# Kernel optimization log

Hardware: AMD Instinct MI355X
Metric: run time of the kernel (lower is better)

## Reference

```python
import jax, jax.numpy as jnp
import numpy as np

SIZES = [(1362944, 123904), (123904, 11264), (11264, 1024)]  # (n_src, n_tgt) per hop
FANOUT = 10
IN_CH, HID, OUT_CH = 128, 256, 47
BN_EPS = 1e-5


def setup_inputs() -> dict:
    key = jax.random.key(0)
    ks = iter(jax.random.split(key, 64))
    inp = {"x": jax.random.normal(next(ks), (SIZES[0][0], IN_CH), jnp.float32)}
    for i, (ns, nt) in enumerate(SIZES):
        e = nt * FANOUT
        src = jax.random.randint(next(ks), (e,), 0, ns, dtype=jnp.int32)
        tgt = jax.random.randint(next(ks), (e,), 0, nt, dtype=jnp.int32)
        inp[f"ei{i}"] = jnp.stack([src, tgt])  # [2, E]
    dins = [IN_CH, HID, HID]
    for i, din in enumerate(dins):
        inp[f"c{i}_w1"] = jax.random.normal(next(ks), (din, HID), jnp.float32) * (2.0 / din) ** 0.5
        inp[f"c{i}_b1"] = jnp.zeros((HID,), jnp.float32)
        inp[f"c{i}_g"] = jnp.ones((HID,), jnp.float32)
        inp[f"c{i}_be"] = jnp.zeros((HID,), jnp.float32)
        inp[f"c{i}_w2"] = jax.random.normal(next(ks), (HID, HID), jnp.float32) * (2.0 / HID) ** 0.5
        inp[f"c{i}_b2"] = jnp.zeros((HID,), jnp.float32)
    inp["lin1_w"] = jax.random.normal(next(ks), (HID, HID), jnp.float32) * (1.0 / HID) ** 0.5
    inp["lin1_b"] = jnp.zeros((HID,), jnp.float32)
    inp["lin2_w"] = jax.random.normal(next(ks), (HID, OUT_CH), jnp.float32) * (1.0 / HID) ** 0.5
    inp["lin2_b"] = jnp.zeros((OUT_CH,), jnp.float32)
    return inp


def _gin_layer(x, ei, n_tgt, w1, b1, g, be, w2, b2):
    # GINConv(eps=0): h = MLP(x_target + sum_{j->i} x_j)
    x_tgt = x[:n_tgt]
    msg = jax.ops.segment_sum(x[ei[0]], ei[1], num_segments=n_tgt)
    h = x_tgt + msg
    h = h @ w1 + b1
    mu = jnp.mean(h, axis=0)
    var = jnp.var(h, axis=0)  # biased, as in torch BN training mode
    h = (h - mu) * jax.lax.rsqrt(var + BN_EPS) * g + be
    h = jax.nn.relu(h)
    h = jax.nn.relu(h @ w2 + b2)
    return h


def reference(x, ei0, ei1, ei2,
              c0_w1, c0_b1, c0_g, c0_be, c0_w2, c0_b2,
              c1_w1, c1_b1, c1_g, c1_be, c1_w2, c1_b2,
              c2_w1, c2_b1, c2_g, c2_be, c2_w2, c2_b2,
              lin1_w, lin1_b, lin2_w, lin2_b):
    eis = [ei0, ei1, ei2]
    params = [(c0_w1, c0_b1, c0_g, c0_be, c0_w2, c0_b2),
              (c1_w1, c1_b1, c1_g, c1_be, c1_w2, c1_b2),
              (c2_w1, c2_b1, c2_g, c2_be, c2_w2, c2_b2)]
    h = x
    for i, (_, n_tgt) in enumerate(SIZES):
        h = _gin_layer(h, eis[i], n_tgt, *params[i])
    h = jax.nn.relu(h @ lin1_w + lin1_b)
    # dropout(p=0.5) is identity in eval mode
    h = h @ lin2_w + lin2_b
    return jax.nn.log_softmax(h, axis=-1)
```

## Files before the change

### kernel.cpp

```cpp
#include <hip/hip_runtime.h>
#include <cmath>

typedef _Float16 f16;
typedef _Float16 half8 __attribute__((ext_vector_type(8)));
typedef _Float16 half4 __attribute__((ext_vector_type(4)));
typedef float f32x4 __attribute__((ext_vector_type(4)));

__device__ __forceinline__ void atomAddF(float* p, float v) { unsafeAtomicAdd(p, v); }

__device__ __forceinline__ void gload16(const void* g, void* l) {
    __builtin_amdgcn_global_load_lds((const __attribute__((address_space(1))) void*)g,
                                     (__attribute__((address_space(3))) void*)l, 16, 0, 0);
}

struct SetupP {
    const float* ws[7];
    f16* wd[7];
    const float* l2s;
    float* l2d;
    float* stats;
    int* deg;
};

__global__ void setup_all(SetupP p) {
    int i = blockIdx.x * 256 + threadIdx.x;
    if (i < 32768) {
        int k = i >> 8, n = i & 255;
        p.wd[0][(size_t)n * 128 + k] = (f16)p.ws[0][i];
        return;
    }
    i -= 32768;
    if (i < 6 * 65536) {
        int m = i >> 16, r = i & 65535;
        int k = r >> 8, n = r & 255;
        p.wd[1 + m][(size_t)n * 256 + k] = (f16)p.ws[1 + m][r];
        return;
    }
    i -= 6 * 65536;
    if (i < 12032) {
        int k = i / 47, j = i - k * 47;
        p.l2d[(size_t)j * 256 + k] = p.l2s[i];
        return;
    }
    i -= 12032;
    if (i < 1536) {
        p.stats[i] = 0.f;
        return;
    }
    i -= 1536;
    if (i < 136192) p.deg[i] = 0;
}

__global__ void fill_all(const int* __restrict__ e0, const int* __restrict__ e1,
                         const int* __restrict__ e2, int E0, int E1, int E2, int* __restrict__ deg,
                         int* __restrict__ adj) {
    int e = blockIdx.x * 256 + threadIdx.x;
    const int *src, *tgt;
    int* d;
    int* a;
    if (e < E0) {
        src = e0; tgt = e0 + E0; d = deg; a = adj;
    } else if (e < E0 + E1) {
        e -= E0;
        src = e1; tgt = e1 + E1; d = deg + 123904; a = adj + (size_t)123904 * 64;
    } else if (e < E0 + E1 + E2) {
        e -= E0 + E1;
        src = e2; tgt = e2 + E2; d = deg + 135168; a = adj + (size_t)135168 * 64;
    } else {
        return;
    }
    int t = tgt[e];
    int pos = atomicAdd(&d[t], 1);
    if (pos < 64) a[(size_t)t * 64 + pos] = src[e];
}


__global__ void gather128(const float* __restrict__ x, const int* __restrict__ deg,
                          const int* __restrict__ adj, f16* __restrict__ h) {
    const int wave = threadIdx.x >> 6, lane = threadIdx.x & 63;
    const int row = blockIdx.x * 4 + wave;
    const int c = lane * 2;
    const float* xr = x + (size_t)row * 128 + c;
    float a0 = xr[0], a1 = xr[1];
    const int n = min(deg[row], 64);
    const int myadj = adj[(size_t)row * 64 + lane];
    int j = 0;
    for (; j + 4 <= n; j += 4) {
        int s0 = __shfl(myadj, j), s1 = __shfl(myadj, j + 1);
        int s2 = __shfl(myadj, j + 2), s3 = __shfl(myadj, j + 3);
        const float* p0 = x + (size_t)s0 * 128 + c;
        const float* p1 = x + (size_t)s1 * 128 + c;
        const float* p2 = x + (size_t)s2 * 128 + c;
        const float* p3 = x + (size_t)s3 * 128 + c;
        float b00 = p0[0], b01 = p0[1], b10 = p1[0], b11 = p1[1];
        float b20 = p2[0], b21 = p2[1], b30 = p3[0], b31 = p3[1];
        a0 += (b00 + b10) + (b20 + b30);
        a1 += (b01 + b11) + (b21 + b31);
    }
    for (; j < n; ++j) {
        int s = __shfl(myadj, j);
        const float* p = x + (size_t)s * 128 + c;
        a0 += p[0];
        a1 += p[1];
    }
    f16* hp = h + (size_t)row * 128 + c;
    hp[0] = (f16)a0;
    hp[1] = (f16)a1;
}

__global__ void gather256(const f16* __restrict__ x, const int* __restrict__ deg,
                          const int* __restrict__ adj, f16* __restrict__ h) {
    const int wave = threadIdx.x >> 6, lane = threadIdx.x & 63;
    const int row = blockIdx.x * 4 + wave;
    const int c = lane * 4;
    half4 xv = *(const half4*)(x + (size_t)row * 256 + c);
    float a0 = (float)xv[0], a1 = (float)xv[1], a2 = (float)xv[2], a3 = (float)xv[3];
    const int n = min(deg[row], 64);
    const int myadj = adj[(size_t)row * 64 + lane];
    int j = 0;
    for (; j + 4 <= n; j += 4) {
        int s0 = __shfl(myadj, j), s1 = __shfl(myadj, j + 1);
        int s2 = __shfl(myadj, j + 2), s3 = __shfl(myadj, j + 3);
        half4 v0 = *(const half4*)(x + (size_t)s0 * 256 + c);
        half4 v1 = *(const half4*)(x + (size_t)s1 * 256 + c);
        half4 v2 = *(const half4*)(x + (size_t)s2 * 256 + c);
        half4 v3 = *(const half4*)(x + (size_t)s3 * 256 + c);
        a0 += ((float)v0[0] + (float)v1[0]) + ((float)v2[0] + (float)v3[0]);
        a1 += ((float)v0[1] + (float)v1[1]) + ((float)v2[1] + (float)v3[1]);
        a2 += ((float)v0[2] + (float)v1[2]) + ((float)v2[2] + (float)v3[2]);
        a3 += ((float)v0[3] + (float)v1[3]) + ((float)v2[3] + (float)v3[3]);
    }
    for (; j < n; ++j) {
        int s = __shfl(myadj, j);
        half4 v = *(const half4*)(x + (size_t)s * 256 + c);
        a0 += (float)v[0];
        a1 += (float)v[1];
        a2 += (float)v[2];
        a3 += (float)v[3];
    }
    half4 o;
    o[0] = (f16)a0;
    o[1] = (f16)a1;
    o[2] = (f16)a2;
    o[3] = (f16)a3;
    *(half4*)(h + (size_t)row * 256 + c) = o;
}

__global__ __launch_bounds__(256) void gemm128_stats(const f16* __restrict__ A,
                                                     const f16* __restrict__ Bt,
                                                     const float* __restrict__ bias,
                                                     f16* __restrict__ C,
                                                     float* __restrict__ colsum,
                                                     float* __restrict__ colsumsq, int M, int N,
                                                     int K) {
    __shared__ __attribute__((aligned(16))) f16 sA[128 * 32];
    __shared__ __attribute__((aligned(16))) f16 sB[128 * 32];
    __shared__ float ssum[128], ssq[128];
    const int tid = threadIdx.x;
    const int wave = tid >> 6, lane = tid & 63;
    const int quad = lane >> 4, l16 = lane & 15;
    const int wr = (wave & 1) * 64, wc = (wave >> 1) * 64;
    const int row0 = blockIdx.x * 128, col0 = blockIdx.y * 128;

    if (tid < 128)
        ssum[tid] = 0.f;
    else
        ssq[tid - 128] = 0.f;

    const int i0 = tid, i1 = tid + 256;
    const int r0s = i0 >> 2, c0s = (i0 & 3) ^ ((r0s >> 1) & 3);
    const int r1s = i1 >> 2, c1s = (i1 & 3) ^ ((r1s >> 1) & 3);
    const f16* ga0 = A + (size_t)(row0 + r0s) * K + c0s * 8;
    const f16* ga1 = A + (size_t)(row0 + r1s) * K + c1s * 8;
    const f16* gb0 = Bt + (size_t)(col0 + r0s) * K + c0s * 8;
    const f16* gb1 = Bt + (size_t)(col0 + r1s) * K + c1s * 8;
    f16* la0 = &sA[i0 * 8];
    f16* la1 = &sA[i1 * 8];
    f16* lb0 = &sB[i0 * 8];
    f16* lb1 = &sB[i1 * 8];

    f32x4 acc[4][4] = {};

    for (int k0 = 0; k0 < K; k0 += 32) {
        __syncthreads();
        gload16(ga0 + k0, la0);
        gload16(ga1 + k0, la1);
        gload16(gb0 + k0, lb0);
        gload16(gb1 + k0, lb1);
        __syncthreads();
        half8 af[4], bf[4];
#pragma unroll
        for (int r = 0; r < 4; ++r) {
            const int ar = wr + r * 16 + l16;
            af[r] = *(const half8*)&sA[ar * 32 + ((quad ^ ((ar >> 1) & 3)) * 8)];
        }
#pragma unroll
        for (int c = 0; c < 4; ++c) {
            const int br = wc + c * 16 + l16;
            bf[c] = *(const half8*)&sB[br * 32 + ((quad ^ ((br >> 1) & 3)) * 8)];
        }
#pragma unroll
        for (int r = 0; r < 4; ++r)
#pragma unroll
            for (int c = 0; c < 4; ++c)
                acc[r][c] = __builtin_amdgcn_mfma_f32_16x16x32_f16(af[r], bf[c], acc[r][c], 0, 0, 0);
    }

#pragma unroll
    for (int c = 0; c < 4; ++c) {
        const int lcol = wc + c * 16 + l16;
        const int gcol = col0 + lcol;
        const float b = bias[gcol];
        float cs = 0.f, cq = 0.f;
#pragma unroll
        for (int r = 0; r < 4; ++r) {
#pragma unroll
            for (int i = 0; i < 4; ++i) {
                const int grow = row0 + wr + r * 16 + quad * 4 + i;
                float v = acc[r][c][i] + b;
                C[(size_t)grow * N + gcol] = (f16)v;
                cs += v;
                cq += v * v;
            }
        }
        cs += __shfl_xor(cs, 16);
        cs += __shfl_xor(cs, 32);
        cq += __shfl_xor(cq, 16);
        cq += __shfl_xor(cq, 32);
        if (quad == 0) {
            atomicAdd(&ssum[lcol], cs);
            atomicAdd(&ssq[lcol], cq);
        }
    }
    __syncthreads();
    if (tid < 128)
        atomAddF(&colsum[col0 + tid], ssum[tid]);
    else
        atomAddF(&colsumsq[col0 + tid - 128], ssq[tid - 128]);
}

__global__ __launch_bounds__(256) void gemm128_bn(const f16* __restrict__ A,
                                                  const f16* __restrict__ Bt,
                                                  const float* __restrict__ bias,
                                                  const float* __restrict__ colsum,
                                                  const float* __restrict__ colsumsq,
                                                  const float* __restrict__ g,
                                                  const float* __restrict__ be, float nt_inv,
                                                  f16* __restrict__ C, int M, int N, int K) {
    __shared__ __attribute__((aligned(16))) f16 sA[128 * 32];
    __shared__ __attribute__((aligned(16))) f16 sB[128 * 32];
    __shared__ float s_scale[256], s_shift[256];
    const int tid = threadIdx.x;
    const int wave = tid >> 6, lane = tid & 63;
    const int quad = lane >> 4, l16 = lane & 15;
    const int wr = (wave & 1) * 64, wc = (wave >> 1) * 64;
    const int row0 = blockIdx.x * 128, col0 = blockIdx.y * 128;

    {
        float mu = colsum[tid] * nt_inv;
        float var = colsumsq[tid] * nt_inv - mu * mu;
        float sc = g[tid] * rsqrtf(var + 1e-5f);
        s_scale[tid] = sc;
        s_shift[tid] = be[tid] - mu * sc;
    }
    __syncthreads();

    const int i0 = tid, i1 = tid + 256;
    const int r0s = i0 >> 2, c0s = (i0 & 3) ^ ((r0s >> 1) & 3);
    const int r1s = i1 >> 2, c1s = (i1 & 3) ^ ((r1s >> 1) & 3);
    const f16* ga0 = A + (size_t)(row0 + r0s) * K + c0s * 8;
    const f16* ga1 = A + (size_t)(row0 + r1s) * K + c1s * 8;
    const f16* gb0 = Bt + (size_t)(col0 + r0s) * K + c0s * 8;
    const f16* gb1 = Bt + (size_t)(col0 + r1s) * K + c1s * 8;
    f16* la0 = &sA[i0 * 8];
    f16* la1 = &sA[i1 * 8];
    f16* lb0 = &sB[i0 * 8];
    f16* lb1 = &sB[i1 * 8];

    f32x4 acc[4][4] = {};

    for (int k0 = 0; k0 < K; k0 += 32) {
        half8 va0 = *(const half8*)(ga0 + k0);
        half8 va1 = *(const half8*)(ga1 + k0);
        half8 ta0, ta1;
        const int kb0 = k0 + c0s * 8, kb1 = k0 + c1s * 8;
#pragma unroll
        for (int j = 0; j < 8; ++j) {
            float f0 = (float)va0[j] * s_scale[kb0 + j] + s_shift[kb0 + j];
            ta0[j] = (f16)fmaxf(f0, 0.f);
            float f1 = (float)va1[j] * s_scale[kb1 + j] + s_shift[kb1 + j];
            ta1[j] = (f16)fmaxf(f1, 0.f);
        }
        __syncthreads();
        gload16(gb0 + k0, lb0);
        gload16(gb1 + k0, lb1);
        *(half8*)la0 = ta0;
        *(half8*)la1 = ta1;
        __syncthreads();
        half8 af[4], bf[4];
#pragma unroll
        for (int r = 0; r < 4; ++r) {
            const int ar = wr + r * 16 + l16;
            af[r] = *(const half8*)&sA[ar * 32 + ((quad ^ ((ar >> 1) & 3)) * 8)];
        }
#pragma unroll
        for (int c = 0; c < 4; ++c) {
            const int br = wc + c * 16 + l16;
            bf[c] = *(const half8*)&sB[br * 32 + ((quad ^ ((br >> 1) & 3)) * 8)];
        }
#pragma unroll
        for (int r = 0; r < 4; ++r)
#pragma unroll
            for (int c = 0; c < 4; ++c)
                acc[r][c] = __builtin_amdgcn_mfma_f32_16x16x32_f16(af[r], bf[c], acc[r][c], 0, 0, 0);
    }

#pragma unroll
    for (int c = 0; c < 4; ++c) {
        const int gcol = col0 + wc + c * 16 + l16;
        const float b = bias[gcol];
#pragma unroll
        for (int r = 0; r < 4; ++r) {
#pragma unroll
            for (int i = 0; i < 4; ++i) {
                const int grow = row0 + wr + r * 16 + quad * 4 + i;
                float v = fmaxf(acc[r][c][i] + b, 0.f);
                C[(size_t)grow * N + gcol] = (f16)v;
            }
        }
    }
}

template <bool RELU>
__global__ __launch_bounds__(256) void gemm_bt(const f16* __restrict__ A, const f16* __restrict__ Bt,
                                               const float* __restrict__ bias, f16* __restrict__ C,
                                               int M, int N, int K) {
    constexpr int BM = 64, BN = 64, BK = 32, LP = 40;
    __shared__ f16 sA[BM * LP];
    __shared__ f16 sB[BN * LP];
    const int tid = threadIdx.x;
    const int wave = tid >> 6, lane = tid & 63;
    const int quad = lane >> 4, l16 = lane & 15;
    const int wr = (wave & 1) * 32, wc = (wave >> 1) * 32;
    const int row0 = blockIdx.x * BM, col0 = blockIdx.y * BN;
    const int srow = tid >> 2, soff = (tid & 3) * 8;

    f32x4 acc[2][2] = {};

    for (int k0 = 0; k0 < K; k0 += BK) {
        __syncthreads();
        *(half8*)&sA[srow * LP + soff] =
            *(const half8*)(A + (size_t)(row0 + srow) * K + (k0 + soff));
        *(half8*)&sB[srow * LP + soff] =
            *(const half8*)(Bt + (size_t)(col0 + srow) * K + (k0 + soff));
        __syncthreads();
        half8 af[2], bf[2];
#pragma unroll
        for (int r = 0; r < 2; ++r) af[r] = *(const half8*)&sA[(wr + r * 16 + l16) * LP + quad * 8];
#pragma unroll
        for (int c = 0; c < 2; ++c) bf[c] = *(const half8*)&sB[(wc + c * 16 + l16) * LP + quad * 8];
#pragma unroll
        for (int r = 0; r < 2; ++r)
#pragma unroll
            for (int c = 0; c < 2; ++c)
                acc[r][c] = __builtin_amdgcn_mfma_f32_16x16x32_f16(af[r], bf[c], acc[r][c], 0, 0, 0);
    }

#pragma unroll
    for (int c = 0; c < 2; ++c) {
        const int gcol = col0 + wc + c * 16 + l16;
        const float b = bias[gcol];
#pragma unroll
        for (int r = 0; r < 2; ++r) {
#pragma unroll
            for (int i = 0; i < 4; ++i) {
                const int grow = row0 + wr + r * 16 + quad * 4 + i;
                float v = acc[r][c][i] + b;
                if (RELU) v = fmaxf(v, 0.f);
                C[(size_t)grow * N + gcol] = (f16)v;
            }
        }
    }
}

__global__ void head2(const f16* __restrict__ T, const float* __restrict__ w2t,
                      const float* __restrict__ b2, float* __restrict__ out, int rows) {
    const int row = blockIdx.x;
    const int lane = threadIdx.x;
    __shared__ float tr[256];
    for (int i = lane; i < 256; i += 64) tr[i] = (float)T[(size_t)row * 256 + i];
    __syncthreads();
    float d = -1e30f;
    if (lane < 47) {
        const float* wr = w2t + (size_t)lane * 256;
        float dot = 0.f;
        for (int k = 0; k < 256; k += 4) {
            dot += tr[k] * wr[k] + tr[k + 1] * wr[k + 1] + tr[k + 2] * wr[k + 2] +
                   tr[k + 3] * wr[k + 3];
        }
        d = dot + b2[lane];
    }
    float m = d;
    for (int off = 32; off; off >>= 1) m = fmaxf(m, __shfl_xor(m, off));
    float e = (lane < 47) ? expf(d - m) : 0.f;
    float s = e;
    for (int off = 32; off; off >>= 1) s += __shfl_xor(s, off);
    if (lane < 47) out[(size_t)row * 47 + lane] = d - m - logf(s);
}


extern "C" void kernel_launch(void* const* d_in, const int* in_sizes, int n_in, void* d_out,
                              int out_size, void* d_ws, size_t ws_size, hipStream_t stream) {
    const float* x0 = (const float*)d_in[0];
    const int* ei[3] = {(const int*)d_in[1], (const int*)d_in[2], (const int*)d_in[3]};
    const int E[3] = {in_sizes[1] / 2, in_sizes[2] / 2, in_sizes[3] / 2};
    const float* c_w1[3] = {(const float*)d_in[4], (const float*)d_in[10], (const float*)d_in[16]};
    const float* c_b1[3] = {(const float*)d_in[5], (const float*)d_in[11], (const float*)d_in[17]};
    const float* c_g[3] = {(const float*)d_in[6], (const float*)d_in[12], (const float*)d_in[18]};
    const float* c_be[3] = {(const float*)d_in[7], (const float*)d_in[13], (const float*)d_in[19]};
    const float* c_w2[3] = {(const float*)d_in[8], (const float*)d_in[14], (const float*)d_in[20]};
    const float* c_b2[3] = {(const float*)d_in[9], (const float*)d_in[15], (const float*)d_in[21]};
    const float* lin1_w = (const float*)d_in[22];
    const float* lin1_b = (const float*)d_in[23];
    const float* lin2_w = (const float*)d_in[24];
    const float* lin2_b = (const float*)d_in[25];
    float* out = (float*)d_out;

    const int NT[3] = {123904, 11264, 1024};

    char* base = (char*)d_ws;
    size_t off = 0;
    auto take = [&](size_t bytes) -> char* {
        char* p = base + off;
        off = (off + bytes + 255) & ~(size_t)255;
        return p;
    };
    f16* w1t[3];
    w1t[0] = (f16*)take((size_t)256 * 128 * sizeof(f16));
    w1t[1] = (f16*)take((size_t)256 * 256 * sizeof(f16));
    w1t[2] = (f16*)take((size_t)256 * 256 * sizeof(f16));
    f16* w2t[3];
    for (int i = 0; i < 3; ++i) w2t[i] = (f16*)take((size_t)256 * 256 * sizeof(f16));
    f16* lin1t = (f16*)take((size_t)256 * 256 * sizeof(f16));
    float* lin2t_ = (float*)take((size_t)47 * 256 * sizeof(float));
    float* stats = (float*)take(3 * 512 * sizeof(float));
    int* deg = (int*)take((size_t)136192 * sizeof(int));
    int* adj = (int*)take((size_t)136192 * 64 * sizeof(int));
    f16* h0 = (f16*)take((size_t)123904 * 128 * sizeof(f16));
    f16* h1 = (f16*)take((size_t)123904 * 256 * sizeof(f16));
    f16* X1 = (f16*)take((size_t)123904 * 256 * sizeof(f16));
    f16* X2 = (f16*)take((size_t)11264 * 256 * sizeof(f16));
    f16* X3 = (f16*)take((size_t)1024 * 256 * sizeof(f16));
    f16* T = (f16*)take((size_t)1024 * 256 * sizeof(f16));
    (void)ws_size;
    (void)out_size;
    (void)n_in;

    int* deg_l[3] = {deg, deg + 123904, deg + 135168};
    int* adj_l[3] = {adj, adj + (size_t)123904 * 64, adj + (size_t)135168 * 64};
    float* cs_l[3] = {stats, stats + 512, stats + 1024};

    SetupP sp;
    sp.ws[0] = c_w1[0];
    sp.ws[1] = c_w1[1];
    sp.ws[2] = c_w1[2];
    sp.ws[3] = c_w2[0];
    sp.ws[4] = c_w2[1];
    sp.ws[5] = c_w2[2];
    sp.ws[6] = lin1_w;
    sp.wd[0] = w1t[0];
    sp.wd[1] = w1t[1];
    sp.wd[2] = w1t[2];
    sp.wd[3] = w2t[0];
    sp.wd[4] = w2t[1];
    sp.wd[5] = w2t[2];
    sp.wd[6] = lin1t;
    sp.l2s = lin2_w;
    sp.l2d = lin2t_;
    sp.stats = stats;
    sp.deg = deg;
    setup_all<<<2249, 256, 0, stream>>>(sp);

    fill_all<<<(E[0] + E[1] + E[2] + 255) / 256, 256, 0, stream>>>(ei[0], ei[1], ei[2], E[0], E[1],
                                                                  E[2], deg, adj);

    gather128<<<NT[0] / 4, 256, 0, stream>>>(x0, deg_l[0], adj_l[0], h0);
    gemm128_stats<<<dim3(NT[0] / 128, 2), 256, 0, stream>>>(h0, w1t[0], c_b1[0], h1, cs_l[0],
                                                            cs_l[0] + 256, NT[0], 256, 128);
    gemm128_bn<<<dim3(NT[0] / 128, 2), 256, 0, stream>>>(h1, w2t[0], c_b2[0], cs_l[0],
                                                         cs_l[0] + 256, c_g[0], c_be[0],
                                                         1.0f / NT[0], X1, NT[0], 256, 256);

    gather256<<<NT[1] / 4, 256, 0, stream>>>(X1, deg_l[1], adj_l[1], h0);
    gemm128_stats<<<dim3(NT[1] / 128, 2), 256, 0, stream>>>(h0, w1t[1], c_b1[1], h1, cs_l[1],
                                                            cs_l[1] + 256, NT[1], 256, 256);
    gemm128_bn<<<dim3(NT[1] / 128, 2), 256, 0, stream>>>(h1, w2t[1], c_b2[1], cs_l[1],
                                                         cs_l[1] + 256, c_g[1], c_be[1],
                                                         1.0f / NT[1], X2, NT[1], 256, 256);

    gather256<<<NT[2] / 4, 256, 0, stream>>>(X2, deg_l[2], adj_l[2], h0);
    gemm128_stats<<<dim3(NT[2] / 128, 2), 256, 0, stream>>>(h0, w1t[2], c_b1[2], h1, cs_l[2],
                                                            cs_l[2] + 256, NT[2], 256, 256);
    gemm128_bn<<<dim3(NT[2] / 128, 2), 256, 0, stream>>>(h1, w2t[2], c_b2[2], cs_l[2],
                                                         cs_l[2] + 256, c_g[2], c_be[2],
                                                         1.0f / NT[2], X3, NT[2], 256, 256);

    gemm_bt<true><<<dim3(16, 4), 256, 0, stream>>>(X3, lin1t, lin1_b, T, 1024, 256, 256);
    head2<<<1024, 64, 0, stream>>>(T, lin2t_, lin2_b, out, 1024);
}
```

Before: 1.191 ms.

## Use full-width 128x256 GEMM tiles with 1024-thread blocks and vectorize gather128

The layer GEMMs now compute the full 256-column output per block with 16 waves instead of two 128x128 tiles per row block. Each A tile is loaded once, and in the BN kernel the A-side normalization is done once instead of twice. gather128 now loads float4 per lane, with the two half-waves handling alternate neighbors, and combines the halves with a cross-lane shuffle. The cost is fewer, larger blocks and fewer accumulators per wave, which may lower latency hiding and occupancy on small layers.

Result: no change. 1.195 ms (+0.3%).

```diff
diff --git a/kernel.cpp b/kernel.cpp
--- a/kernel.cpp
+++ b/kernel.cpp
@@ -79,33 +79,51 @@
                           const int* __restrict__ adj, f16* __restrict__ h) {
     const int wave = threadIdx.x >> 6, lane = threadIdx.x & 63;
     const int row = blockIdx.x * 4 + wave;
-    const int c = lane * 2;
-    const float* xr = x + (size_t)row * 128 + c;
-    float a0 = xr[0], a1 = xr[1];
+    const int hf = lane >> 5;
+    const int c = (lane & 31) * 4;
+    float a0 = 0.f, a1 = 0.f, a2 = 0.f, a3 = 0.f;
+    if (hf == 0) {
+        f32x4 v = *(const f32x4*)(x + (size_t)row * 128 + c);
+        a0 = v[0]; a1 = v[1]; a2 = v[2]; a3 = v[3];
+    }
     const int n = min(deg[row], 64);
     const int myadj = adj[(size_t)row * 64 + lane];
     int j = 0;
     for (; j + 4 <= n; j += 4) {
-        int s0 = __shfl(myadj, j), s1 = __shfl(myadj, j + 1);
-        int s2 = __shfl(myadj, j + 2), s3 = __shfl(myadj, j + 3);
-        const float* p0 = x + (size_t)s0 * 128 + c;
-        const float* p1 = x + (size_t)s1 * 128 + c;
-        const float* p2 = x + (size_t)s2 * 128 + c;
-        const float* p3 = x + (size_t)s3 * 128 + c;
-        float b00 = p0[0], b01 = p0[1], b10 = p1[0], b11 = p1[1];
-        float b20 = p2[0], b21 = p2[1], b30 = p3[0], b31 = p3[1];
-        a0 += (b00 + b10) + (b20 + b30);
-        a1 += (b01 + b11) + (b21 + b31);
-    }
-    for (; j < n; ++j) {
-        int s = __shfl(myadj, j);
-        const float* p = x + (size_t)s * 128 + c;
-        a0 += p[0];
-        a1 += p[1];
-    }
-    f16* hp = h + (size_t)row * 128 + c;
-    hp[0] = (f16)a0;
-    hp[1] = (f16)a1;
+        int sA = __shfl(myadj, j + hf);
+        int sB = __shfl(myadj, j + 2 + hf);
+        f32x4 vA = *(const f32x4*)(x + (size_t)sA * 128 + c);
+        f32x4 vB = *(const f32x4*)(x + (size_t)sB * 128 + c);
+        a0 += vA[0] + vB[0];
+        a1 += vA[1] + vB[1];
+        a2 += vA[2] + vB[2];
+        a3 += vA[3] + vB[3];
+    }
+    {
+        const int i0 = j + hf, i1 = j + 2 + hf;
+        int s0 = __shfl(myadj, i0 & 63);
+        int s1 = __shfl(myadj, i1 & 63);
+        if (i0 < n) {
+            f32x4 v = *(const f32x4*)(x + (size_t)s0 * 128 + c);
+            a0 += v[0]; a1 += v[1]; a2 += v[2]; a3 += v[3];
+        }
+        if (i1 < n) {
+            f32x4 v = *(const f32x4*)(x + (size_t)s1 * 128 + c);
+            a0 += v[0]; a1 += v[1]; a2 += v[2]; a3 += v[3];
+        }
+    }
+    a0 += __shfl_xor(a0, 32);
+    a1 += __shfl_xor(a1, 32);
+    a2 += __shfl_xor(a2, 32);
+    a3 += __shfl_xor(a3, 32);
+    if (hf == 0) {
+        half4 o;
+        o[0] = (f16)a0;
+        o[1] = (f16)a1;
+        o[2] = (f16)a2;
+        o[3] = (f16)a3;
+        *(half4*)(h + (size_t)row * 128 + c) = o;
+    }
 }
 
 __global__ void gather256(const f16* __restrict__ x, const int* __restrict__ deg,
@@ -146,51 +164,44 @@
     *(half4*)(h + (size_t)row * 256 + c) = o;
 }
 
-__global__ __launch_bounds__(256) void gemm128_stats(const f16* __restrict__ A,
+__global__ __launch_bounds__(1024) void gemmFW_stats(const f16* __restrict__ A,
                                                      const f16* __restrict__ Bt,
                                                      const float* __restrict__ bias,
                                                      f16* __restrict__ C,
                                                      float* __restrict__ colsum,
-                                                     float* __restrict__ colsumsq, int M, int N,
-                                                     int K) {
+                                                     float* __restrict__ colsumsq, int M, int K) {
     __shared__ __attribute__((aligned(16))) f16 sA[128 * 32];
-    __shared__ __attribute__((aligned(16))) f16 sB[128 * 32];
-    __shared__ float ssum[128], ssq[128];
+    __shared__ __attribute__((aligned(16))) f16 sB[256 * 32];
+    __shared__ float ssum[256], ssq[256];
     const int tid = threadIdx.x;
-    const int wave = tid >> 6, lane = tid & 63;
+    const int wid = tid >> 6, lane = tid & 63;
     const int quad = lane >> 4, l16 = lane & 15;
-    const int wr = (wave & 1) * 64, wc = (wave >> 1) * 64;
-    const int row0 = blockIdx.x * 128, col0 = blockIdx.y * 128;
-
-    if (tid < 128)
+    const int wr = (wid & 3) * 32, wc = (wid >> 2) * 64;
+    const int row0 = blockIdx.x * 128;
+
+    if (tid < 256) {
         ssum[tid] = 0.f;
-    else
-        ssq[tid - 128] = 0.f;
-
-    const int i0 = tid, i1 = tid + 256;
-    const int r0s = i0 >> 2, c0s = (i0 & 3) ^ ((r0s >> 1) & 3);
-    const int r1s = i1 >> 2, c1s = (i1 & 3) ^ ((r1s >> 1) & 3);
-    const f16* ga0 = A + (size_t)(row0 + r0s) * K + c0s * 8;
-    const f16* ga1 = A + (size_t)(row0 + r1s) * K + c1s * 8;
-    const f16* gb0 = Bt + (size_t)(col0 + r0s) * K + c0s * 8;
-    const f16* gb1 = Bt + (size_t)(col0 + r1s) * K + c1s * 8;
-    f16* la0 = &sA[i0 * 8];
-    f16* la1 = &sA[i1 * 8];
-    f16* lb0 = &sB[i0 * 8];
-    f16* lb1 = &sB[i1 * 8];
-
-    f32x4 acc[4][4] = {};
+        ssq[tid] = 0.f;
+    }
+
+    const int rb = tid >> 2, cb = (tid & 3) ^ ((rb >> 1) & 3);
+    const f16* gB = Bt + (size_t)rb * K + cb * 8;
+    f16* lB = &sB[tid * 8];
+    const int ia = tid & 511;
+    const int ra = ia >> 2, ca = (ia & 3) ^ ((ra >> 1) & 3);
+    const f16* gA = A + (size_t)(row0 + ra) * K + ca * 8;
+    f16* lA = &sA[ia * 8];
+
+    f32x4 acc[2][4] = {};
 
     for (int k0 = 0; k0 < K; k0 += 32) {
         __syncthreads();
-        gload16(ga0 + k0, la0);
-        gload16(ga1 + k0, la1);
-        gload16(gb0 + k0, lb0);
-        gload16(gb1 + k0, lb1);
+        gload16(gB + k0, lB);
+        if (tid < 512) gload16(gA + k0, lA);
         __syncthreads();
-        half8 af[4], bf[4];
-#pragma unroll
-        for (int r = 0; r < 4; ++r) {
+        half8 af[2], bf[4];
+#pragma unroll
+        for (int r = 0; r < 2; ++r) {
             const int ar = wr + r * 16 + l16;
             af[r] = *(const half8*)&sA[ar * 32 + ((quad ^ ((ar >> 1) & 3)) * 8)];
         }
@@ -200,7 +211,7 @@
             bf[c] = *(const half8*)&sB[br * 32 + ((quad ^ ((br >> 1) & 3)) * 8)];
         }
 #pragma unroll
-        for (int r = 0; r < 4; ++r)
+        for (int r = 0; r < 2; ++r)
 #pragma unroll
             for (int c = 0; c < 4; ++c)
                 acc[r][c] = __builtin_amdgcn_mfma_f32_16x16x32_f16(af[r], bf[c], acc[r][c], 0, 0, 0);
@@ -209,16 +220,15 @@
 #pragma unroll
     for (int c = 0; c < 4; ++c) {
         const int lcol = wc + c * 16 + l16;
-        const int gcol = col0 + lcol;
-        const float b = bias[gcol];
+        const float b = bias[lcol];
         float cs = 0.f, cq = 0.f;
 #pragma unroll
-        for (int r = 0; r < 4; ++r) {
+        for (int r = 0; r < 2; ++r) {
 #pragma unroll
             for (int i = 0; i < 4; ++i) {
                 const int grow = row0 + wr + r * 16 + quad * 4 + i;
                 float v = acc[r][c][i] + b;
-                C[(size_t)grow * N + gcol] = (f16)v;
+                C[(size_t)grow * 256 + lcol] = (f16)v;
                 cs += v;
                 cq += v * v;
             }
@@ -233,30 +243,30 @@
         }
     }
     __syncthreads();
-    if (tid < 128)
-        atomAddF(&colsum[col0 + tid], ssum[tid]);
-    else
-        atomAddF(&colsumsq[col0 + tid - 128], ssq[tid - 128]);
-}
-
-__global__ __launch_bounds__(256) void gemm128_bn(const f16* __restrict__ A,
+    if (tid < 256)
+        atomAddF(&colsum[tid], ssum[tid]);
+    else if (tid < 512)
+        atomAddF(&colsumsq[tid - 256], ssq[tid - 256]);
+}
+
+__global__ __launch_bounds__(1024) void gemmFW_bn(const f16* __restrict__ A,
                                                   const f16* __restrict__ Bt,
                                                   const float* __restrict__ bias,
                                                   const float* __restrict__ colsum,
                                                   const float* __restrict__ colsumsq,
                                                   const float* __restrict__ g,
                                                   const float* __restrict__ be, float nt_inv,
-                                                  f16* __restrict__ C, int M, int N, int K) {
+                                                  f16* __restrict__ C, int M, int K) {
     __shared__ __attribute__((aligned(16))) f16 sA[128 * 32];
-    __shared__ __attribute__((aligned(16))) f16 sB[128 * 32];
+    __shared__ __attribute__((aligned(16))) f16 sB[256 * 32];
     __shared__ float s_scale[256], s_shift[256];
     const int tid = threadIdx.x;
-    const int wave = tid >> 6, lane = tid & 63;
+    const int wid = tid >> 6, lane = tid & 63;
     const int quad = lane >> 4, l16 = lane & 15;
-    const int wr = (wave & 1) * 64, wc = (wave >> 1) * 64;
-    const int row0 = blockIdx.x * 128, col0 = blockIdx.y * 128;
-
-    {
+    const int wr = (wid & 3) * 32, wc = (wid >> 2) * 64;
+    const int row0 = blockIdx.x * 128;
+
+    if (tid < 256) {
         float mu = colsum[tid] * nt_inv;
         float var = colsumsq[tid] * nt_inv - mu * mu;
         float sc = g[tid] * rsqrtf(var + 1e-5f);
@@ -265,41 +275,34 @@
     }
     __syncthreads();
 
-    const int i0 = tid, i1 = tid + 256;
-    const int r0s = i0 >> 2, c0s = (i0 & 3) ^ ((r0s >> 1) & 3);
-    const int r1s = i1 >> 2, c1s = (i1 & 3) ^ ((r1s >> 1) & 3);
-    const f16* ga0 = A + (size_t)(row0 + r0s) * K + c0s * 8;
-    const f16* ga1 = A + (size_t)(row0 + r1s) * K + c1s * 8;
-    const f16* gb0 = Bt + (size_t)(col0 + r0s) * K + c0s * 8;
-    const f16* gb1 = Bt + (size_t)(col0 + r1s) * K + c1s * 8;
-    f16* la0 = &sA[i0 * 8];
-    f16* la1 = &sA[i1 * 8];
-    f16* lb0 = &sB[i0 * 8];
-    f16* lb1 = &sB[i1 * 8];
-
-    f32x4 acc[4][4] = {};
+    const int rb = tid >> 2, cb = (tid & 3) ^ ((rb >> 1) & 3);
+    const f16* gB = Bt + (size_t)rb * K + cb * 8;
+    f16* lB = &sB[tid * 8];
+    const int ia = tid & 511;
+    const int ra = ia >> 2, ca = (ia & 3) ^ ((ra >> 1) & 3);
+    const f16* gA = A + (size_t)(row0 + ra) * K + ca * 8;
+    f16* lA = &sA[ia * 8];
+
+    f32x4 acc[2][4] = {};
 
     for (int k0 = 0; k0 < K; k0 += 32) {
-        half8 va0 = *(const half8*)(ga0 + k0);
-        half8 va1 = *(const half8*)(ga1 + k0);
-        half8 ta0, ta1;
-        const int kb0 = k0 + c0s * 8, kb1 = k0 + c1s * 8;
-#pragma unroll
-        for (int j = 0; j < 8; ++j) {
-            float f0 = (float)va0[j] * s_scale[kb0 + j] + s_shift[kb0 + j];
-            ta0[j] = (f16)fmaxf(f0, 0.f);
-            float f1 = (float)va1[j] * s_scale[kb1 + j] + s_shift[kb1 + j];
-            ta1[j] = (f16)fmaxf(f1, 0.f);
+        half8 ta;
+        if (tid < 512) {
+            half8 va = *(const half8*)(gA + k0);
+            const int kb = k0 + ca * 8;
+#pragma unroll
+            for (int j = 0; j < 8; ++j) {
+                float f = (float)va[j] * s_scale[kb + j] + s_shift[kb + j];
+                ta[j] = (f16)fmaxf(f, 0.f);
+            }
         }
         __syncthreads();
-        gload16(gb0 + k0, lb0);
-        gload16(gb1 + k0, lb1);
-        *(half8*)la0 = ta0;
-        *(half8*)la1 = ta1;
+        gload16(gB + k0, lB);
+        if (tid < 512) *(half8*)lA = ta;
         __syncthreads();
-        half8 af[4], bf[4];
-#pragma unroll
-        for (int r = 0; r < 4; ++r) {
+        half8 af[2], bf[4];
+#pragma unroll
+        for (int r = 0; r < 2; ++r) {
             const int ar = wr + r * 16 + l16;
             af[r] = *(const half8*)&sA[ar * 32 + ((quad ^ ((ar >> 1) & 3)) * 8)];
         }
@@ -309,7 +312,7 @@
             bf[c] = *(const half8*)&sB[br * 32 + ((quad ^ ((br >> 1) & 3)) * 8)];
         }
 #pragma unroll
-        for (int r = 0; r < 4; ++r)
+        for (int r = 0; r < 2; ++r)
 #pragma unroll
             for (int c = 0; c < 4; ++c)
                 acc[r][c] = __builtin_amdgcn_mfma_f32_16x16x32_f16(af[r], bf[c], acc[r][c], 0, 0, 0);
@@ -317,15 +320,15 @@
 
 #pragma unroll
     for (int c = 0; c < 4; ++c) {
-        const int gcol = col0 + wc + c * 16 + l16;
-        const float b = bias[gcol];
-#pragma unroll
-        for (int r = 0; r < 4; ++r) {
+        const int lcol = wc + c * 16 + l16;
+        const float b = bias[lcol];
+#pragma unroll
+        for (int r = 0; r < 2; ++r) {
 #pragma unroll
             for (int i = 0; i < 4; ++i) {
                 const int grow = row0 + wr + r * 16 + quad * 4 + i;
                 float v = fmaxf(acc[r][c][i] + b, 0.f);
-                C[(size_t)grow * N + gcol] = (f16)v;
+                C[(size_t)grow * 256 + lcol] = (f16)v;
             }
         }
     }
@@ -485,25 +488,22 @@
                                                                   E[2], deg, adj);
 
     gather128<<<NT[0] / 4, 256, 0, stream>>>(x0, deg_l[0], adj_l[0], h0);
-    gemm128_stats<<<dim3(NT[0] / 128, 2), 256, 0, stream>>>(h0, w1t[0], c_b1[0], h1, cs_l[0],
-                                                            cs_l[0] + 256, NT[0], 256, 128);
-    gemm128_bn<<<dim3(NT[0] / 128, 2), 256, 0, stream>>>(h1, w2t[0], c_b2[0], cs_l[0],
-                                                         cs_l[0] + 256, c_g[0], c_be[0],
-                                                         1.0f / NT[0], X1, NT[0], 256, 256);
+    gemmFW_stats<<<NT[0] / 128, 1024, 0, stream>>>(h0, w1t[0], c_b1[0], h1, cs_l[0], cs_l[0] + 256,
+                                                   NT[0], 128);
+    gemmFW_bn<<<NT[0] / 128, 1024, 0, stream>>>(h1, w2t[0], c_b2[0], cs_l[0], cs_l[0] + 256,
+                                                c_g[0], c_be[0], 1.0f / NT[0], X1, NT[0], 256);
 
     gather256<<<NT[1] / 4, 256, 0, stream>>>(X1, deg_l[1], adj_l[1], h0);
-    gemm128_stats<<<dim3(NT[1] / 128, 2), 256, 0, stream>>>(h0, w1t[1], c_b1[1], h1, cs_l[1],
-                                                            cs_l[1] + 256, NT[1], 256, 256);
-    gemm128_bn<<<dim3(NT[1] / 128, 2), 256, 0, stream>>>(h1, w2t[1], c_b2[1], cs_l[1],
-                                                         cs_l[1] + 256, c_g[1], c_be[1],
-                                                         1.0f / NT[1], X2, NT[1], 256, 256);
+    gemmFW_stats<<<NT[1] / 128, 1024, 0, stream>>>(h0, w1t[1], c_b1[1], h1, cs_l[1], cs_l[1] + 256,
+                                                   NT[1], 256);
+    gemmFW_bn<<<NT[1] / 128, 1024, 0, stream>>>(h1, w2t[1], c_b2[1], cs_l[1], cs_l[1] + 256,
+                                                c_g[1], c_be[1], 1.0f / NT[1], X2, NT[1], 256);
 
     gather256<<<NT[2] / 4, 256, 0, stream>>>(X2, deg_l[2], adj_l[2], h0);
-    gemm128_stats<<<dim3(NT[2] / 128, 2), 256, 0, stream>>>(h0, w1t[2], c_b1[2], h1, cs_l[2],
-                                                            cs_l[2] + 256, NT[2], 256, 256);
-    gemm128_bn<<<dim3(NT[2] / 128, 2), 256, 0, stream>>>(h1, w2t[2], c_b2[2], cs_l[2],
-                                                         cs_l[2] + 256, c_g[2], c_be[2],
-                                                         1.0f / NT[2], X3, NT[2], 256, 256);
+    gemmFW_stats<<<NT[2] / 128, 1024, 0, stream>>>(h0, w1t[2], c_b1[2], h1, cs_l[2], cs_l[2] + 256,
+                                                   NT[2], 256);
+    gemmFW_bn<<<NT[2] / 128, 1024, 0, stream>>>(h1, w2t[2], c_b2[2], cs_l[2], cs_l[2] + 256,
+                                                c_g[2], c_be[2], 1.0f / NT[2], X3, NT[2], 256);
 
     gemm_bt<true><<<dim3(16, 4), 256, 0, stream>>>(X3, lin1t, lin1_b, T, 1024, 256, 256);
     head2<<<1024, 64, 0, stream>>>(T, lin2t_, lin2_b, out, 1024);
```
